# Kernel optimization log

Measured on AMD Instinct MI355X. Metric: run time of the kernel, lower is better.

## Reference

```python
import jax, jax.numpy as jnp
import numpy as np

H = 8          # num_heads
DK = 64        # head dim (head_size // num_heads)
SPARSITY = 0.5 # pre-softmax random drop probability
DROPOUT = 0.1  # post-softmax dropout probability


def setup_inputs() -> dict:
    key = jax.random.key(0)
    ks = jax.random.split(key, 12)
    B, S, D = 4, 2048, 512
    mk = lambda k, shp, scale=1.0: (jax.random.normal(k, shp, dtype=jnp.float32) * scale)
    return {
        "query": mk(ks[0], (B, S, D)),
        "key": mk(ks[1], (B, S, D)),
        "value": mk(ks[2], (B, S, D)),
        "Wq": mk(ks[3], (D, D), 0.04),
        "bq": mk(ks[4], (D,), 0.02),
        "Wk": mk(ks[5], (D, D), 0.04),
        "bk": mk(ks[6], (D,), 0.02),
        "Wv": mk(ks[7], (D, D), 0.04),
        "bv": mk(ks[8], (D,), 0.02),
        "Wo": mk(ks[9], (D, D), 0.04),
        "bo": mk(ks[10], (D,), 0.02),
    }


def _split_heads(x, B):
    # [B, S, H*DK] -> [B, H, S, DK]
    return x.reshape(B, -1, H, DK).transpose(0, 2, 1, 3)


def reference(query, key, value, Wq, bq, Wk, bk, Wv, bv, Wo, bo):
    B, S, D = query.shape
    # q/k/v projections (torch Linear: x @ W.T + b)
    q = _split_heads(query @ Wq.T + bq, B)   # [B, H, S, DK]
    k = _split_heads(key @ Wk.T + bk, B)
    v = _split_heads(value @ Wv.T + bv, B)

    scores = jnp.einsum("bhqd,bhkd->bhqk", q, k) / jnp.sqrt(jnp.float32(DK))

    # random pre-softmax sparsity mask: keep where U(0,1) > sparsity
    mkey = jax.random.fold_in(jax.random.key(42), 1)
    keep_sparse = jax.random.uniform(mkey, scores.shape) > SPARSITY
    scores = jnp.where(keep_sparse, scores, -jnp.inf)

    p_attn = jax.nn.softmax(scores, axis=-1)

    # dropout on attention probs, inverted scaling as in torch
    dkey = jax.random.fold_in(jax.random.key(42), 2)
    keep_drop = jax.random.uniform(dkey, p_attn.shape) >= DROPOUT
    p_attn = jnp.where(keep_drop, p_attn / (1.0 - DROPOUT), 0.0)

    x = jnp.einsum("bhqk,bhkd->bhqd", p_attn, v)        # [B, H, S, DK]
    x = x.transpose(0, 2, 1, 3).reshape(B, S, H * DK)    # [B, S, D]
    return x @ Wo.T + bo
```

## Files before the change

### kernel.cpp

```cpp
#include <hip/hip_runtime.h>
#include <stdint.h>

#define BATCH  4
#define SQ     2048
#define DMODEL 512
#define NH     8
#define DK     64

typedef __attribute__((ext_vector_type(8))) short short8;
typedef __attribute__((ext_vector_type(4))) float f32x4;

__device__ __forceinline__ void tf2x32(uint32_t k0, uint32_t k1,
                                       uint32_t x0, uint32_t x1,
                                       uint32_t &o0, uint32_t &o1) {
  const uint32_t ks2 = k0 ^ k1 ^ 0x1BD11BDAu;
  x0 += k0; x1 += k1;
#define TFR(d) { x0 += x1; x1 = (x1 << (d)) | (x1 >> (32 - (d))); x1 ^= x0; }
  TFR(13) TFR(15) TFR(26) TFR(6)
  x0 += k1; x1 += ks2 + 1u;
  TFR(17) TFR(29) TFR(16) TFR(24)
  x0 += ks2; x1 += k0 + 2u;
  TFR(13) TFR(15) TFR(26) TFR(6)
  x0 += k0; x1 += k1 + 3u;
  TFR(17) TFR(29) TFR(16) TFR(24)
  x0 += k1; x1 += ks2 + 4u;
  TFR(13) TFR(15) TFR(26) TFR(6)
  x0 += ks2; x1 += k0 + 5u;
#undef TFR
  o0 = x0; o1 = x1;
}

__device__ __forceinline__ float u01(uint32_t bits) {
  return __uint_as_float((bits >> 9) | 0x3f800000u) - 1.0f;
}

__device__ __forceinline__ ushort f2bf_rne(float f) {
  uint32_t u = __float_as_uint(f);
  return (ushort)((u + 0x7fffu + ((u >> 16) & 1u)) >> 16);
}

__global__ __launch_bounds__(256) void mask_kernel(uint32_t *__restrict__ sp,
                                                   uint32_t *__restrict__ dp) {
  uint32_t w = blockIdx.x * 256u + threadIdx.x;
  uint32_t s0, s1, d0, d1;
  tf2x32(0u, 42u, 0u, 1u, s0, s1);
  tf2x32(0u, 42u, 0u, 2u, d0, d1);
  uint32_t base = w * 32u;
  uint32_t sw = 0u, dw = 0u;
#pragma unroll 4
  for (int t = 0; t < 32; ++t) {
    uint32_t i = base + (uint32_t)t;
    uint32_t a0, a1;
    tf2x32(s0, s1, 0u, i, a0, a1);
    if (u01(a0 ^ a1) > 0.5f) sw |= (1u << t);
    tf2x32(d0, d1, 0u, i, a0, a1);
    if (u01(a0 ^ a1) >= 0.1f) dw |= (1u << t);
  }
  sp[w] = sw;
  dp[w] = dw;
}

#define BM 64
#define BN 64
#define BK 32
template <int MODE>
__global__ __launch_bounds__(256) void proj_gemm_t(const float *__restrict__ X,
                                                   const float *__restrict__ W,
                                                   const float *__restrict__ bias,
                                                   void *__restrict__ Yv) {
  __shared__ __align__(16) uint8_t smem[17408];
  float (*Xs)[BM + 4] = (float (*)[BM + 4])smem;
  float (*Ws)[BN + 4] = (float (*)[BN + 4])(smem + 8704);
  const int bm = blockIdx.y * BM;
  const int bn = blockIdx.x * BN;
  const int tid = threadIdx.x;
  const int tx = tid & 15, ty = tid >> 4;
  float acc[4][4] = {};
  const int kk = tid & 31;
  const int r0 = tid >> 5;
  for (int k0 = 0; k0 < DMODEL; k0 += BK) {
#pragma unroll
    for (int p = 0; p < 8; ++p) {
      int r = r0 + p * 8;
      Xs[kk][r] = X[(size_t)(bm + r) * DMODEL + k0 + kk];
      Ws[kk][r] = W[(size_t)(bn + r) * DMODEL + k0 + kk];
    }
    __syncthreads();
#pragma unroll
    for (int k = 0; k < BK; ++k) {
      float4 a = *reinterpret_cast<const float4 *>(&Xs[k][ty * 4]);
      float4 b = *reinterpret_cast<const float4 *>(&Ws[k][tx * 4]);
      float av[4] = {a.x, a.y, a.z, a.w};
      float bv[4] = {b.x, b.y, b.z, b.w};
#pragma unroll
      for (int i = 0; i < 4; ++i)
#pragma unroll
        for (int j = 0; j < 4; ++j) acc[i][j] += av[i] * bv[j];
    }
    __syncthreads();
  }

  if (MODE == 0) {
    float *Y = (float *)Yv;
#pragma unroll
    for (int i = 0; i < 4; ++i) {
      const int m = bm + ty * 4 + i;
#pragma unroll
      for (int j = 0; j < 4; ++j) {
        const int n = bn + tx * 4 + j;
        Y[(size_t)m * DMODEL + n] = acc[i][j] + bias[n];
      }
    }
  } else if (MODE == 1) {
    ushort *Y = (ushort *)Yv;
#pragma unroll
    for (int i = 0; i < 4; ++i) {
      const int m = bm + ty * 4 + i;
      uint32_t u0 = f2bf_rne(acc[i][0] + bias[bn + tx * 4 + 0]);
      uint32_t u1 = f2bf_rne(acc[i][1] + bias[bn + tx * 4 + 1]);
      uint32_t u2 = f2bf_rne(acc[i][2] + bias[bn + tx * 4 + 2]);
      uint32_t u3 = f2bf_rne(acc[i][3] + bias[bn + tx * 4 + 3]);
      uint2 pk;
      pk.x = u0 | (u1 << 16);
      pk.y = u2 | (u3 << 16);
      *(uint2 *)&Y[(size_t)m * DMODEL + bn + tx * 4] = pk;
    }
  } else {
    ushort *T = (ushort *)smem;
#pragma unroll
    for (int i = 0; i < 4; ++i)
#pragma unroll
      for (int j = 0; j < 4; ++j) {
        const int nl = tx * 4 + j, ml = ty * 4 + i;
        T[nl * 72 + ml] = f2bf_rne(acc[i][j] + bias[bn + nl]);
      }
    __syncthreads();
    ushort *Y = (ushort *)Yv;
    const int row = tid >> 2, seg = tid & 3;
    uint4 a = *(uint4 *)&T[row * 72 + seg * 16];
    uint4 b2 = *(uint4 *)&T[row * 72 + seg * 16 + 8];
    const size_t gaddr =
        ((size_t)((bm >> 11) * 512 + bn + row)) * SQ + (bm & 2047) + seg * 16;
    *(uint4 *)&Y[gaddr] = a;
    *(uint4 *)&Y[gaddr + 8] = b2;
  }
}

__global__ __launch_bounds__(256, 4) void attn_mfma(
    const ushort *__restrict__ qp, const ushort *__restrict__ kp,
    const ushort *__restrict__ vpt, const uint32_t *__restrict__ spb,
    const uint32_t *__restrict__ dpb, float *__restrict__ xa) {
  __shared__ __align__(16) uint8_t lds[24576];
  uint8_t *Ks = lds;
  uint8_t *Vt = lds + 8192;
  const int b = blockIdx.z, h = blockIdx.y;
  const int qb = blockIdx.x * 64;
  const int tid = threadIdx.x;
  const int w = tid >> 6, l = tid & 63;
  const int lr = l & 15, lq = l >> 4;
  uint8_t *Ps = lds + 16384 + w * 2048;
  const int bh = b * NH + h;

  short8 qf[2];
  {
    const int qrow = qb + w * 16 + lr;
    const ushort *qrowp = qp + ((size_t)(b * SQ + qrow)) * DMODEL + h * DK;
    qf[0] = *(const short8 *)(qrowp + lq * 8);
    qf[1] = *(const short8 *)(qrowp + 32 + lq * 8);
  }
  f32x4 o[4];
  f32x4 lacc;
#pragma unroll
  for (int nd = 0; nd < 4; ++nd) o[nd] = (f32x4){0.f, 0.f, 0.f, 0.f};
  lacc = (f32x4){0.f, 0.f, 0.f, 0.f};

  for (int kv = 0; kv < SQ; kv += 64) {
    __syncthreads();
    {
      const int row = tid >> 2;
      const int c0 = (tid & 3) * 2;
      const int sw = (row & 7) << 4;
      const ushort *ksrc =
          kp + ((size_t)(b * SQ + kv + row)) * DMODEL + h * DK + c0 * 8;
      uint4 d0 = *(const uint4 *)ksrc;
      uint4 d1 = *(const uint4 *)(ksrc + 8);
      *(uint4 *)(Ks + ((row * 128 + c0 * 16) ^ sw)) = d0;
      *(uint4 *)(Ks + ((row * 128 + (c0 + 1) * 16) ^ sw)) = d1;
      const ushort *vsrc = vpt + ((size_t)(bh * DK + row)) * SQ + kv + c0 * 8;
      uint4 e0 = *(const uint4 *)vsrc;
      uint4 e1 = *(const uint4 *)(vsrc + 8);
      *(uint4 *)(Vt + ((row * 128 + c0 * 16) ^ sw)) = e0;
      *(uint4 *)(Vt + ((row * 128 + (c0 + 1) * 16) ^ sw)) = e1;
    }
    __syncthreads();

    f32x4 s[4];
#pragma unroll
    for (int ni = 0; ni < 4; ++ni) s[ni] = (f32x4){0.f, 0.f, 0.f, 0.f};
#pragma unroll
    for (int ni = 0; ni < 4; ++ni) {
      const int krow = ni * 16 + lr;
      const int sw = (krow & 7) << 4;
#pragma unroll
      for (int kf = 0; kf < 2; ++kf) {
        short8 kb =
            *(const short8 *)(Ks + ((krow * 128 + kf * 64 + lq * 16) ^ sw));
        s[ni] = __builtin_amdgcn_mfma_f32_16x16x32_bf16(qf[kf], kb, s[ni], 0, 0, 0);
      }
    }

    const int wq = kv >> 5;
    const size_t mbase = ((size_t)bh * SQ + (qb + w * 16 + lq * 4)) * 64 + wq;
    uint2 swd[4], dwd[4];
#pragma unroll
    for (int r = 0; r < 4; ++r) {
      swd[r] = *(const uint2 *)(spb + mbase + (size_t)r * 64);
      dwd[r] = *(const uint2 *)(dpb + mbase + (size_t)r * 64);
    }

#pragma unroll
    for (int ni = 0; ni < 4; ++ni) {
      const int bpos = (ni & 1) * 16 + lr;
#pragma unroll
      for (int r = 0; r < 4; ++r) {
        const uint32_t sws = (ni < 2) ? swd[r].x : swd[r].y;
        const uint32_t dws = (ni < 2) ? dwd[r].x : dwd[r].y;
        float e = __expf(s[ni][r] * 0.125f);
        float p = ((sws >> bpos) & 1u) ? e : 0.0f;
        lacc[r] += p;
        float pd = ((dws >> bpos) & 1u) ? p * (1.0f / 0.9f) : 0.0f;
        const int prow = lq * 4 + r;
        *(ushort *)(Ps + ((prow * 128 + (ni * 16 + lr) * 2) ^ ((prow & 7) << 4))) =
            f2bf_rne(pd);
      }
    }

#pragma unroll
    for (int kf = 0; kf < 2; ++kf) {
      short8 pa = *(const short8 *)(Ps +
                                    ((lr * 128 + kf * 64 + lq * 16) ^ ((lr & 7) << 4)));
#pragma unroll
      for (int nd = 0; nd < 4; ++nd) {
        const int vrow = nd * 16 + lr;
        short8 vb = *(const short8 *)(Vt + ((vrow * 128 + kf * 64 + lq * 16) ^
                                            ((vrow & 7) << 4)));
        o[nd] = __builtin_amdgcn_mfma_f32_16x16x32_bf16(pa, vb, o[nd], 0, 0, 0);
      }
    }
  }

  float inv[4];
#pragma unroll
  for (int r = 0; r < 4; ++r) {
    float t = lacc[r];
    t += __shfl_xor(t, 1);
    t += __shfl_xor(t, 2);
    t += __shfl_xor(t, 4);
    t += __shfl_xor(t, 8);
    inv[r] = 1.0f / t;
  }
#pragma unroll
  for (int nd = 0; nd < 4; ++nd)
#pragma unroll
    for (int r = 0; r < 4; ++r) {
      const int qrow = qb + w * 16 + lq * 4 + r;
      xa[((size_t)(b * SQ + qrow)) * DMODEL + h * DK + nd * 16 + lr] =
          o[nd][r] * inv[r];
    }
}

extern "C" void kernel_launch(void *const *d_in, const int *in_sizes, int n_in,
                              void *d_out, int out_size, void *d_ws,
                              size_t ws_size, hipStream_t stream) {
  (void)in_sizes; (void)n_in; (void)out_size;
  const float *query = (const float *)d_in[0];
  const float *key_  = (const float *)d_in[1];
  const float *value = (const float *)d_in[2];
  const float *Wq = (const float *)d_in[3];
  const float *bq = (const float *)d_in[4];
  const float *Wk = (const float *)d_in[5];
  const float *bk = (const float *)d_in[6];
  const float *Wv = (const float *)d_in[7];
  const float *bv = (const float *)d_in[8];
  const float *Wo = (const float *)d_in[9];
  const float *bo = (const float *)d_in[10];
  float *out = (float *)d_out;

  const size_t MB = (size_t)1 << 20;
  if (ws_size < 72 * MB) return;

  char *ws = (char *)d_ws;
  ushort *qp  = (ushort *)(ws);
  ushort *kp  = (ushort *)(ws + 8 * MB);
  ushort *vpt = (ushort *)(ws + 16 * MB);
  float  *xa  = (float *)(ws + 24 * MB);
  uint32_t *spb = (uint32_t *)(ws + 40 * MB);
  uint32_t *dpb = (uint32_t *)(ws + 56 * MB);

  mask_kernel<<<16384, 256, 0, stream>>>(spb, dpb);

  dim3 gg(DMODEL / BN, (BATCH * SQ) / BM);
  proj_gemm_t<1><<<gg, 256, 0, stream>>>(query, Wq, bq, (void *)qp);
  proj_gemm_t<1><<<gg, 256, 0, stream>>>(key_, Wk, bk, (void *)kp);
  proj_gemm_t<2><<<gg, 256, 0, stream>>>(value, Wv, bv, (void *)vpt);

  attn_mfma<<<dim3(SQ / 64, NH, BATCH), 256, 0, stream>>>(qp, kp, vpt, spb,
                                                          dpb, xa);

  proj_gemm_t<0><<<gg, 256, 0, stream>>>(xa, Wo, bo, out);
}
```

Measured before the change: 872.0 us.

## Fuse Threefry mask generation into attention kernel, drop mask buffers

Removes the separate mask kernel that wrote 32 MB of packed keep-bits and instead computes the Threefry random bits inline in the attention kernel, per score element. The key schedule is folded at compile time and the rotations use alignbit, with float comparisons replaced by integer thresholds. This trades mask-buffer memory traffic and a kernel launch for a lot of extra integer ALU work inside the attention loop. Launch bounds are relaxed from 4 to 2 blocks per SIMD to give the hash more registers, which may lower occupancy.

```diff
diff --git a/kernel.cpp b/kernel.cpp
--- a/kernel.cpp
+++ b/kernel.cpp
@@ -10,54 +10,52 @@
 typedef __attribute__((ext_vector_type(8))) short short8;
 typedef __attribute__((ext_vector_type(4))) float f32x4;
 
-__device__ __forceinline__ void tf2x32(uint32_t k0, uint32_t k1,
-                                       uint32_t x0, uint32_t x1,
-                                       uint32_t &o0, uint32_t &o1) {
-  const uint32_t ks2 = k0 ^ k1 ^ 0x1BD11BDAu;
+struct TFK { uint32_t a, b; };
+constexpr uint32_t rotl_ce(uint32_t x, int d) {
+  return (x << d) | (x >> (32 - d));
+}
+constexpr TFK tf_ce(uint32_t k0, uint32_t k1, uint32_t x0, uint32_t x1) {
+  const uint32_t ks[3] = {k0, k1, k0 ^ k1 ^ 0x1BD11BDAu};
+  const int rot[2][4] = {{13, 15, 26, 6}, {17, 29, 16, 24}};
   x0 += k0; x1 += k1;
-#define TFR(d) { x0 += x1; x1 = (x1 << (d)) | (x1 >> (32 - (d))); x1 ^= x0; }
-  TFR(13) TFR(15) TFR(26) TFR(6)
-  x0 += k1; x1 += ks2 + 1u;
-  TFR(17) TFR(29) TFR(16) TFR(24)
-  x0 += ks2; x1 += k0 + 2u;
-  TFR(13) TFR(15) TFR(26) TFR(6)
-  x0 += k0; x1 += k1 + 3u;
-  TFR(17) TFR(29) TFR(16) TFR(24)
-  x0 += k1; x1 += ks2 + 4u;
-  TFR(13) TFR(15) TFR(26) TFR(6)
-  x0 += ks2; x1 += k0 + 5u;
-#undef TFR
-  o0 = x0; o1 = x1;
-}
-
-__device__ __forceinline__ float u01(uint32_t bits) {
-  return __uint_as_float((bits >> 9) | 0x3f800000u) - 1.0f;
-}
+  for (int c = 0; c < 5; ++c) {
+    for (int j = 0; j < 4; ++j) {
+      x0 += x1; x1 = rotl_ce(x1, rot[c & 1][j]); x1 ^= x0;
+    }
+    x0 += ks[(c + 1) % 3];
+    x1 += ks[(c + 2) % 3] + (uint32_t)(c + 1);
+  }
+  return TFK{x0, x1};
+}
+constexpr TFK SPK = tf_ce(0u, 42u, 0u, 1u);
+constexpr TFK DPK = tf_ce(0u, 42u, 0u, 2u);
+
+template <uint32_t K0, uint32_t K1>
+__device__ __forceinline__ uint32_t tf_bits(uint32_t ctr) {
+  constexpr uint32_t KS2 = K0 ^ K1 ^ 0x1BD11BDAu;
+  uint32_t x0 = K0;
+  uint32_t x1 = K1 + ctr;
+#define RND(d) { x0 += x1; x1 = __builtin_amdgcn_alignbit(x1, x1, 32 - (d)); x1 ^= x0; }
+  RND(13) RND(15) RND(26) RND(6)
+  x0 += K1; x1 += KS2 + 1u;
+  RND(17) RND(29) RND(16) RND(24)
+  x0 += KS2; x1 += K0 + 2u;
+  RND(13) RND(15) RND(26) RND(6)
+  x0 += K0; x1 += K1 + 3u;
+  RND(17) RND(29) RND(16) RND(24)
+  x0 += K1; x1 += KS2 + 4u;
+  RND(13) RND(15) RND(26) RND(6)
+  x0 += KS2; x1 += K0 + 5u;
+#undef RND
+  return x0 ^ x1;
+}
+
+#define SP_THR 0x80000200u
+#define DP_THR 0x1999A200u
 
 __device__ __forceinline__ ushort f2bf_rne(float f) {
   uint32_t u = __float_as_uint(f);
   return (ushort)((u + 0x7fffu + ((u >> 16) & 1u)) >> 16);
-}
-
-__global__ __launch_bounds__(256) void mask_kernel(uint32_t *__restrict__ sp,
-                                                   uint32_t *__restrict__ dp) {
-  uint32_t w = blockIdx.x * 256u + threadIdx.x;
-  uint32_t s0, s1, d0, d1;
-  tf2x32(0u, 42u, 0u, 1u, s0, s1);
-  tf2x32(0u, 42u, 0u, 2u, d0, d1);
-  uint32_t base = w * 32u;
-  uint32_t sw = 0u, dw = 0u;
-#pragma unroll 4
-  for (int t = 0; t < 32; ++t) {
-    uint32_t i = base + (uint32_t)t;
-    uint32_t a0, a1;
-    tf2x32(s0, s1, 0u, i, a0, a1);
-    if (u01(a0 ^ a1) > 0.5f) sw |= (1u << t);
-    tf2x32(d0, d1, 0u, i, a0, a1);
-    if (u01(a0 ^ a1) >= 0.1f) dw |= (1u << t);
-  }
-  sp[w] = sw;
-  dp[w] = dw;
 }
 
 #define BM 64
@@ -146,10 +144,9 @@
   }
 }
 
-__global__ __launch_bounds__(256, 4) void attn_mfma(
+__global__ __launch_bounds__(256, 2) void attn_mfma(
     const ushort *__restrict__ qp, const ushort *__restrict__ kp,
-    const ushort *__restrict__ vpt, const uint32_t *__restrict__ spb,
-    const uint32_t *__restrict__ dpb, float *__restrict__ xa) {
+    const ushort *__restrict__ vpt, float *__restrict__ xa) {
   __shared__ __align__(16) uint8_t lds[24576];
   uint8_t *Ks = lds;
   uint8_t *Vt = lds + 8192;
@@ -173,6 +170,11 @@
 #pragma unroll
   for (int nd = 0; nd < 4; ++nd) o[nd] = (f32x4){0.f, 0.f, 0.f, 0.f};
   lacc = (f32x4){0.f, 0.f, 0.f, 0.f};
+
+  uint32_t rowflat[4];
+#pragma unroll
+  for (int r = 0; r < 4; ++r)
+    rowflat[r] = ((uint32_t)(bh * SQ + qb + w * 16 + lq * 4 + r)) << 11;
 
   for (int kv = 0; kv < SQ; kv += 64) {
     __syncthreads();
@@ -209,26 +211,17 @@
       }
     }
 
-    const int wq = kv >> 5;
-    const size_t mbase = ((size_t)bh * SQ + (qb + w * 16 + lq * 4)) * 64 + wq;
-    uint2 swd[4], dwd[4];
-#pragma unroll
-    for (int r = 0; r < 4; ++r) {
-      swd[r] = *(const uint2 *)(spb + mbase + (size_t)r * 64);
-      dwd[r] = *(const uint2 *)(dpb + mbase + (size_t)r * 64);
-    }
-
 #pragma unroll
     for (int ni = 0; ni < 4; ++ni) {
-      const int bpos = (ni & 1) * 16 + lr;
 #pragma unroll
       for (int r = 0; r < 4; ++r) {
-        const uint32_t sws = (ni < 2) ? swd[r].x : swd[r].y;
-        const uint32_t dws = (ni < 2) ? dwd[r].x : dwd[r].y;
+        const uint32_t ctr = rowflat[r] + (uint32_t)(kv + ni * 16 + lr);
+        const bool keep_s = tf_bits<SPK.a, SPK.b>(ctr) >= SP_THR;
+        const bool keep_d = tf_bits<DPK.a, DPK.b>(ctr) >= DP_THR;
         float e = __expf(s[ni][r] * 0.125f);
-        float p = ((sws >> bpos) & 1u) ? e : 0.0f;
+        float p = keep_s ? e : 0.0f;
         lacc[r] += p;
-        float pd = ((dws >> bpos) & 1u) ? p * (1.0f / 0.9f) : 0.0f;
+        float pd = keep_d ? p * (1.0f / 0.9f) : 0.0f;
         const int prow = lq * 4 + r;
         *(ushort *)(Ps + ((prow * 128 + (ni * 16 + lr) * 2) ^ ((prow & 7) << 4))) =
             f2bf_rne(pd);
@@ -287,25 +280,20 @@
   float *out = (float *)d_out;
 
   const size_t MB = (size_t)1 << 20;
-  if (ws_size < 72 * MB) return;
+  if (ws_size < 40 * MB) return;
 
   char *ws = (char *)d_ws;
   ushort *qp  = (ushort *)(ws);
   ushort *kp  = (ushort *)(ws + 8 * MB);
   ushort *vpt = (ushort *)(ws + 16 * MB);
   float  *xa  = (float *)(ws + 24 * MB);
-  uint32_t *spb = (uint32_t *)(ws + 40 * MB);
-  uint32_t *dpb = (uint32_t *)(ws + 56 * MB);
-
-  mask_kernel<<<16384, 256, 0, stream>>>(spb, dpb);
 
   dim3 gg(DMODEL / BN, (BATCH * SQ) / BM);
   proj_gemm_t<1><<<gg, 256, 0, stream>>>(query, Wq, bq, (void *)qp);
   proj_gemm_t<1><<<gg, 256, 0, stream>>>(key_, Wk, bk, (void *)kp);
   proj_gemm_t<2><<<gg, 256, 0, stream>>>(value, Wv, bv, (void *)vpt);
 
-  attn_mfma<<<dim3(SQ / 64, NH, BATCH), 256, 0, stream>>>(qp, kp, vpt, spb,
-                                                          dpb, xa);
+  attn_mfma<<<dim3(SQ / 64, NH, BATCH), 256, 0, stream>>>(qp, kp, vpt, xa);
 
   proj_gemm_t<0><<<gg, 256, 0, stream>>>(xa, Wo, bo, out);
 }
```

Measured after the change: 794.0 us. 9.0% less time.
